# Kernel optimization log

Measured on AMD Instinct MI355X. Metric: run time of the kernel, lower is better.

Reference implementation:

```python
import jax, jax.numpy as jnp
import numpy as np

B, S, H = 2, 2048, 2048
NH, KVH, HD = 16, 4, 128
R = 16
LORA_SCALE = 32.0 / 16.0  # lora_alpha / lora_r
ATTN_SCALE = HD ** -0.5
NEG = -1e9


def setup_inputs() -> dict:
    key = jax.random.key(0)
    ks = jax.random.split(key, 16)
    q_dim, kv_dim = NH * HD, KVH * HD
    # RoPE tables
    inv_freq = 1.0 / (10000.0 ** (jnp.arange(0, HD, 2, dtype=jnp.float32) / HD))
    ang = jnp.arange(S, dtype=jnp.float32)[:, None] * inv_freq[None, :]  # [S, HD/2]
    emb = jnp.concatenate([ang, ang], axis=-1)  # [S, HD]
    cos = jnp.broadcast_to(jnp.cos(emb)[None], (B, S, HD))
    sin = jnp.broadcast_to(jnp.sin(emb)[None], (B, S, HD))
    # additive causal mask [B,1,S,S]
    causal = jnp.triu(jnp.full((S, S), NEG, dtype=jnp.float32), k=1)
    attention_mask = jnp.broadcast_to(causal[None, None], (B, 1, S, S))
    return {
        'hidden_states': jax.random.normal(ks[0], (B, S, H), jnp.float32),
        'cos': cos,
        'sin': sin,
        'attention_mask': attention_mask,
        'q_w': jax.random.normal(ks[1], (q_dim, H), jnp.float32) * 0.02,
        'k_w': jax.random.normal(ks[2], (kv_dim, H), jnp.float32) * 0.02,
        'v_w': jax.random.normal(ks[3], (kv_dim, H), jnp.float32) * 0.02,
        'q_b': jax.random.normal(ks[4], (q_dim,), jnp.float32) * 0.02,
        'k_b': jax.random.normal(ks[5], (kv_dim,), jnp.float32) * 0.02,
        'v_b': jax.random.normal(ks[6], (kv_dim,), jnp.float32) * 0.02,
        'q_A': jax.random.normal(ks[7], (H, R), jnp.float32) * (1.0 / np.sqrt(H)),
        'q_B': jax.random.normal(ks[8], (R, q_dim), jnp.float32) * 0.02,
        'k_A': jax.random.normal(ks[9], (H, R), jnp.float32) * (1.0 / np.sqrt(H)),
        'k_B': jax.random.normal(ks[10], (R, kv_dim), jnp.float32) * 0.02,
        'v_A': jax.random.normal(ks[11], (H, R), jnp.float32) * (1.0 / np.sqrt(H)),
        'v_B': jax.random.normal(ks[12], (R, kv_dim), jnp.float32) * 0.02,
        'o_w': jax.random.normal(ks[13], (H, H), jnp.float32) * 0.02,
    }


def _rotate_half(x):
    x1, x2 = x[..., : HD // 2], x[..., HD // 2:]
    return jnp.concatenate([-x2, x1], axis=-1)


def reference(hidden_states, cos, sin, attention_mask,
              q_w, k_w, v_w, q_b, k_b, v_b,
              q_A, q_B, k_A, k_B, v_A, v_B, o_w):
    x = hidden_states  # dropout p=0 (eval)
    # fused base + LoRA projections
    q = x @ q_w.T + q_b + LORA_SCALE * ((x @ q_A) @ q_B)  # [B,S,NH*HD]
    k = x @ k_w.T + k_b + LORA_SCALE * ((x @ k_A) @ k_B)  # [B,S,KVH*HD]
    v = x @ v_w.T + v_b + LORA_SCALE * ((x @ v_A) @ v_B)
    q = q.reshape(B, S, NH, HD).transpose(0, 2, 1, 3)   # [B,NH,S,HD]
    k = k.reshape(B, S, KVH, HD).transpose(0, 2, 1, 3)  # [B,KVH,S,HD]
    v = v.reshape(B, S, KVH, HD).transpose(0, 2, 1, 3)
    # RoPE
    c = cos[:, None]  # [B,1,S,HD]
    s = sin[:, None]
    q = q * c + _rotate_half(q) * s
    k = k * c + _rotate_half(k) * s
    # GQA: repeat kv heads
    n_rep = NH // KVH
    k = jnp.repeat(k, n_rep, axis=1)  # [B,NH,S,HD]
    v = jnp.repeat(v, n_rep, axis=1)
    scores = jnp.einsum('bhqd,bhkd->bhqk', q, k) * ATTN_SCALE
    scores = scores + attention_mask
    attn = jax.nn.softmax(scores.astype(jnp.float32), axis=-1).astype(q.dtype)
    out = jnp.einsum('bhqk,bhkd->bhqd', attn, v)
    out = out.transpose(0, 2, 1, 3).reshape(B, S, NH * HD)  # [B,S,H]
    return out @ o_w.T
```

## Files before the change

### kernel.cpp

```cpp
#include <hip/hip_runtime.h>

constexpr int cB   = 2;
constexpr int cS   = 2048;
constexpr int cH   = 2048;
constexpr int cNH  = 16;
constexpr int cKVH = 4;
constexpr int cHD  = 128;
constexpr int cQD  = 2048;
constexpr int cKVD = 512;
constexpr int cNQKV = 3072;
constexpr int cNTOK = 4096;
#define ATTN_SCALE 0.08838834764831845f
#define QSCALE 0.12751589549581288f

typedef __bf16 bf16;
typedef __attribute__((ext_vector_type(8))) __bf16 bf16x8;
typedef __attribute__((ext_vector_type(4))) __bf16 bf16x4;
typedef __attribute__((ext_vector_type(4))) float  f32x4;

__device__ __forceinline__ void async_load16(const bf16* g, bf16* l) {
    __builtin_amdgcn_global_load_lds(
        (const __attribute__((address_space(1))) void*)g,
        (__attribute__((address_space(3))) void*)l, 16, 0, 0);
}

__global__ void conv_f32_bf16(const float* __restrict__ in, bf16* __restrict__ out) {
    int i = (blockIdx.x * 256 + threadIdx.x) * 4;
    f32x4 v = *(const f32x4*)(in + i);
    bf16x4 o;
    o[0] = (bf16)v[0]; o[1] = (bf16)v[1]; o[2] = (bf16)v[2]; o[3] = (bf16)v[3];
    *(bf16x4*)(out + i) = o;
}

__global__ __launch_bounds__(256) void prep_w2(
        const float* __restrict__ qw, const float* __restrict__ kw, const float* __restrict__ vw,
        const float* __restrict__ qA, const float* __restrict__ qB,
        const float* __restrict__ kA, const float* __restrict__ kB,
        const float* __restrict__ vA, const float* __restrict__ vB,
        const float* __restrict__ qb, const float* __restrict__ kbias, const float* __restrict__ vb,
        bf16* __restrict__ Wc, float* __restrict__ biasc) {
    const int wave = threadIdx.x >> 6, lane = threadIdx.x & 63;
    const int n = blockIdx.y * 4 + wave;
    const int k0 = blockIdx.x * 512 + lane * 8;
    const float* W; const float* Am; const float* Bm; const float* bias; int nn, nd;
    if (n < cQD)             { W = qw; Am = qA; Bm = qB; bias = qb;    nn = n;               nd = cQD; }
    else if (n < cQD + cKVD) { W = kw; Am = kA; Bm = kB; bias = kbias; nn = n - cQD;         nd = cKVD; }
    else                     { W = vw; Am = vA; Bm = vB; bias = vb;    nn = n - cQD - cKVD;  nd = cKVD; }
    if (blockIdx.x == 0 && lane == 0) biasc[n] = bias[nn];
    float bm[16];
    #pragma unroll
    for (int r = 0; r < 16; ++r) bm[r] = Bm[r * nd + nn];
    const float* wrow = W + (size_t)nn * cH + k0;
    f32x4 w0 = *(const f32x4*)(wrow);
    f32x4 w1 = *(const f32x4*)(wrow + 4);
    bf16x8 o;
    #pragma unroll
    for (int j = 0; j < 8; ++j) {
        const f32x4* am = (const f32x4*)(Am + (size_t)(k0 + j) * 16);
        f32x4 a0 = am[0], a1 = am[1], a2 = am[2], a3 = am[3];
        float acc = 0.f;
        #pragma unroll
        for (int c = 0; c < 4; ++c) acc += a0[c] * bm[c] + a1[c] * bm[4 + c]
                                         + a2[c] * bm[8 + c] + a3[c] * bm[12 + c];
        const float wv = (j < 4) ? w0[j] : w1[j - 4];
        o[j] = (bf16)(wv + 2.0f * acc);
    }
    *(bf16x8*)&Wc[(size_t)n * cH + k0] = o;
}

__global__ __launch_bounds__(512, 2) void gemm_qkv2(const bf16* __restrict__ A, const bf16* __restrict__ Bw,
                                                    const float* __restrict__ bias,
                                                    const float* __restrict__ cosb, const float* __restrict__ sinb,
                                                    bf16* __restrict__ Qr, bf16* __restrict__ Kr,
                                                    bf16* __restrict__ Vt) {
    __shared__ bf16 Al[2][256 * 64];
    __shared__ bf16 Bl[2][256 * 64];
    const int tid = threadIdx.x;
    const int wave = tid >> 6, lane = tid & 63;
    const int quad = lane >> 4, l16 = lane & 15;
    const int wm = wave >> 2, wn = wave & 3;
    const int K = cH;
    constexpr int GX = cNQKV / 256;
    constexpr int NWG = GX * (cNTOK / 256);

    const int orig = blockIdx.y * GX + blockIdx.x;
    const int swz = (orig & 7) * (NWG >> 3) + (orig >> 3);
    const long bm = (long)(swz / GX) * 256;
    const long bn = (long)(swz % GX) * 256;

    f32x4 acc[8][4];
    #pragma unroll
    for (int i = 0; i < 8; ++i)
        #pragma unroll
        for (int j = 0; j < 4; ++j) acc[i][j] = f32x4{0.f, 0.f, 0.f, 0.f};

    int ago[4], slo[4];
    #pragma unroll
    for (int i2 = 0; i2 < 4; ++i2) {
        const int si = i2 * 512 + tid;
        const int row = si >> 3, c8 = si & 7;
        ago[i2] = row * K + (c8 ^ (row & 7)) * 8;
        slo[i2] = si * 8;
    }
    const size_t bmK = (size_t)bm * K, bnK = (size_t)bn * K;

    auto STAGE = [&](int tt, int bb) {
        const bf16* As_ = A  + bmK + (size_t)tt * 64;
        const bf16* Bs_ = Bw + bnK + (size_t)tt * 64;
        #pragma unroll
        for (int i2 = 0; i2 < 4; ++i2) {
            async_load16(As_ + ago[i2], &Al[bb][slo[i2]]);
            async_load16(Bs_ + ago[i2], &Bl[bb][slo[i2]]);
        }
    };

    constexpr int NT = cH / 64;
    STAGE(0, 0);
    STAGE(1, 1);
    const int sw = l16 & 7;
    const int arow = wm * 128 + l16;
    const int brow = (wn >> 1) * 128 + (wn & 1) * 32 + l16;

    for (int t = 0; t < NT; ++t) {
        const int buf = t & 1;
        if (t + 1 < NT) asm volatile("s_waitcnt vmcnt(8)" ::: "memory");
        else            asm volatile("s_waitcnt vmcnt(0)" ::: "memory");
        __builtin_amdgcn_s_barrier();
        const bf16* Ab = &Al[buf][0];
        const bf16* Bb = &Bl[buf][0];
        #pragma unroll
        for (int ih = 0; ih < 2; ++ih) {
            bf16x8 af[4][2];
            #pragma unroll
            for (int ii = 0; ii < 4; ++ii)
                #pragma unroll
                for (int ks = 0; ks < 2; ++ks)
                    af[ii][ks] = *(const bf16x8*)&Ab[(arow + (ih * 4 + ii) * 16) * 64 + (((ks * 4 + quad) ^ sw) * 8)];
            #pragma unroll
            for (int jh = 0; jh < 2; ++jh) {
                bf16x8 bfr[2][2];
                #pragma unroll
                for (int jj = 0; jj < 2; ++jj)
                    #pragma unroll
                    for (int ks = 0; ks < 2; ++ks)
                        bfr[jj][ks] = *(const bf16x8*)&Bb[(brow + jj * 16 + jh * 64) * 64 + (((ks * 4 + quad) ^ sw) * 8)];
                __builtin_amdgcn_s_setprio(1);
                #pragma unroll
                for (int ii = 0; ii < 4; ++ii)
                    #pragma unroll
                    for (int jj = 0; jj < 2; ++jj)
                        #pragma unroll
                        for (int ks = 0; ks < 2; ++ks)
                            acc[ih * 4 + ii][jh * 2 + jj] = __builtin_amdgcn_mfma_f32_16x16x32_bf16(
                                af[ii][ks], bfr[jj][ks], acc[ih * 4 + ii][jh * 2 + jj], 0, 0, 0);
                __builtin_amdgcn_s_setprio(0);
            }
        }
        asm volatile("s_waitcnt lgkmcnt(0)" ::: "memory");
        __builtin_amdgcn_s_barrier();
        if (t + 2 < NT) STAGE(t + 2, buf);
    }

    #pragma unroll
    for (int j = 0; j < 4; ++j) {
        const int nloc = (wn >> 1) * 128 + (wn & 1) * 32 + (j & 1) * 16 + (j >> 1) * 64 + l16;
        const float bv = bias[bn + nloc];
        #pragma unroll
        for (int i = 0; i < 8; ++i)
            #pragma unroll
            for (int r = 0; r < 4; ++r) acc[i][j][r] += bv;
    }

    const int head = (int)(bn >> 7) + (wn >> 1);
    if (head < cNH + cKVH) {
        const bool isQ = head < cNH;
        #pragma unroll
        for (int jlo = 0; jlo < 2; ++jlo) {
            const int d = (wn & 1) * 32 + jlo * 16 + l16;
            #pragma unroll
            for (int i = 0; i < 8; ++i)
                #pragma unroll
                for (int r = 0; r < 4; ++r) {
                    const long tok = bm + wm * 128 + i * 16 + quad * 4 + r;
                    const float cv = cosb[tok * cHD + d];
                    const float sv = sinb[tok * cHD + d];
                    const float v1 = acc[i][jlo][r], v2 = acc[i][jlo + 2][r];
                    float o1 = v1 * cv - v2 * sv;
                    float o2 = v2 * cv + v1 * sv;
                    if (isQ) { o1 *= QSCALE; o2 *= QSCALE; }
                    const int b = (int)(tok >> 11), s = (int)(tok & 2047);
                    bf16* dst = isQ
                        ? Qr + ((size_t)(b * cNH + head) * cS + s) * cHD
                        : Kr + ((size_t)(b * cKVH + (head - cNH)) * cS + s) * cHD;
                    dst[d]      = (bf16)o1;
                    dst[d + 64] = (bf16)o2;
                }
        }
    } else {
        const int kv = head - cNH - cKVH;
        const int b = (int)(bm >> 11);
        const int sbase = (int)(bm & 2047);
        #pragma unroll
        for (int j = 0; j < 4; ++j) {
            const int d = (wn & 1) * 32 + (j & 1) * 16 + (j >> 1) * 64 + l16;
            #pragma unroll
            for (int i = 0; i < 8; ++i) {
                const int s0 = sbase + wm * 128 + i * 16 + quad * 4;
                bf16x4 o4;
                #pragma unroll
                for (int r = 0; r < 4; ++r) o4[r] = (bf16)acc[i][j][r];
                *(bf16x4*)&Vt[((size_t)((b * cKVH + kv) * cHD) + d) * cS + s0] = o4;
            }
        }
    }
}

__global__ __launch_bounds__(512, 2) void gemm_oproj(const bf16* __restrict__ A, const bf16* __restrict__ Bw,
                                                     float* __restrict__ Cp) {
    __shared__ bf16 Al[2][256 * 64];
    __shared__ bf16 Bl[2][128 * 64];
    const int tid = threadIdx.x;
    const int wave = tid >> 6, lane = tid & 63;
    const int quad = lane >> 4, l16 = lane & 15;
    const int wm = wave >> 2, wn = wave & 3;
    constexpr int K = cH, N = cH;
    constexpr int GX = cH / 128;
    constexpr int NWG = GX * (cNTOK / 256);

    const int orig = blockIdx.y * GX + blockIdx.x;
    const int swz = (orig & 7) * (NWG >> 3) + (orig >> 3);
    const long bm = (long)(swz / GX) * 256;
    const long bn = (long)(swz % GX) * 128;

    f32x4 acc[8][2];
    #pragma unroll
    for (int i = 0; i < 8; ++i)
        #pragma unroll
        for (int j = 0; j < 2; ++j) acc[i][j] = f32x4{0.f, 0.f, 0.f, 0.f};

    int ago[4], aslo[4], bgo[2], bslo[2];
    #pragma unroll
    for (int i2 = 0; i2 < 4; ++i2) {
        const int si = i2 * 512 + tid;
        const int row = si >> 3, c8 = si & 7;
        ago[i2] = row * K + (c8 ^ (row & 7)) * 8;
        aslo[i2] = si * 8;
    }
    #pragma unroll
    for (int i2 = 0; i2 < 2; ++i2) {
        const int si = i2 * 512 + tid;
        const int row = si >> 3, c8 = si & 7;
        bgo[i2] = row * K + (c8 ^ (row & 7)) * 8;
        bslo[i2] = si * 8;
    }
    const size_t bmK = (size_t)bm * K, bnK = (size_t)bn * K;

    auto STAGE = [&](int tt, int bb) {
        const bf16* As_ = A  + bmK + (size_t)tt * 64;
        const bf16* Bs_ = Bw + bnK + (size_t)tt * 64;
        #pragma unroll
        for (int i2 = 0; i2 < 4; ++i2) async_load16(As_ + ago[i2], &Al[bb][aslo[i2]]);
        #pragma unroll
        for (int i2 = 0; i2 < 2; ++i2) async_load16(Bs_ + bgo[i2], &Bl[bb][bslo[i2]]);
    };

    constexpr int NT = K / 64;
    STAGE(0, 0);
    STAGE(1, 1);
    const int sw = l16 & 7;
    const int arow = wm * 128 + l16;
    const int brow = wn * 32 + l16;

    for (int t = 0; t < NT; ++t) {
        const int buf = t & 1;
        if (t + 1 < NT) asm volatile("s_waitcnt vmcnt(6)" ::: "memory");
        else            asm volatile("s_waitcnt vmcnt(0)" ::: "memory");
        __builtin_amdgcn_s_barrier();
        const bf16* Ab = &Al[buf][0];
        const bf16* Bb = &Bl[buf][0];
        bf16x8 bfr[2][2];
        #pragma unroll
        for (int jj = 0; jj < 2; ++jj)
            #pragma unroll
            for (int ks = 0; ks < 2; ++ks)
                bfr[jj][ks] = *(const bf16x8*)&Bb[(brow + jj * 16) * 64 + (((ks * 4 + quad) ^ sw) * 8)];
        #pragma unroll
        for (int ih = 0; ih < 2; ++ih) {
            bf16x8 af[4][2];
            #pragma unroll
            for (int ii = 0; ii < 4; ++ii)
                #pragma unroll
                for (int ks = 0; ks < 2; ++ks)
                    af[ii][ks] = *(const bf16x8*)&Ab[(arow + (ih * 4 + ii) * 16) * 64 + (((ks * 4 + quad) ^ sw) * 8)];
            __builtin_amdgcn_s_setprio(1);
            #pragma unroll
            for (int ii = 0; ii < 4; ++ii)
                #pragma unroll
                for (int jj = 0; jj < 2; ++jj)
                    #pragma unroll
                    for (int ks = 0; ks < 2; ++ks)
                        acc[ih * 4 + ii][jj] = __builtin_amdgcn_mfma_f32_16x16x32_bf16(
                            af[ii][ks], bfr[jj][ks], acc[ih * 4 + ii][jj], 0, 0, 0);
            __builtin_amdgcn_s_setprio(0);
        }
        asm volatile("s_waitcnt lgkmcnt(0)" ::: "memory");
        __builtin_amdgcn_s_barrier();
        if (t + 2 < NT) STAGE(t + 2, buf);
    }

    #pragma unroll
    for (int i = 0; i < 8; ++i)
        #pragma unroll
        for (int j = 0; j < 2; ++j) {
            const long m0 = bm + wm * 128 + i * 16 + quad * 4;
            const long n  = bn + wn * 32 + j * 16 + l16;
            #pragma unroll
            for (int r = 0; r < 4; ++r)
                Cp[(m0 + r) * N + n] = acc[i][j][r];
        }
}

__global__ __launch_bounds__(256, 2) void flash4(const bf16* __restrict__ Q, const bf16* __restrict__ K,
                                                 const bf16* __restrict__ Vt, bf16* __restrict__ Ob) {
    __shared__ bf16 kb[8192];
    __shared__ bf16 vb[8192];
    __shared__ bf16 pb[4096];
    const int tid = threadIdx.x;
    const int wave = tid >> 6, lane = tid & 63;
    const int quad = lane >> 4, l16 = lane & 15;
    const int pi = blockIdx.x;
    const int h = blockIdx.y, b = blockIdx.z;

    const bf16* Qh = Q  + (size_t)(b * cNH + h) * cS * cHD;
    const bf16* Kg = K  + (size_t)(b * cKVH + (h >> 2)) * cS * cHD;
    const bf16* Vg = Vt + (size_t)(b * cKVH + (h >> 2)) * cHD * cS;

    int kgo[4], vgo[4], slo[4];
    #pragma unroll
    for (int i2 = 0; i2 < 4; ++i2) {
        const int si = i2 * 256 + tid;
        const int krow = si >> 4, kcsw = si & 15;
        const int kc = (kcsw & 8) | ((kcsw & 7) ^ (krow & 7));
        kgo[i2] = krow * cHD + kc * 8;
        const int vrow = si >> 3, vcsw = si & 7;
        const int vc = vcsw ^ (vrow & 7);
        vgo[i2] = vrow * cS + vc * 8;
        slo[i2] = si * 8;
    }

    #pragma unroll
    for (int t2 = 0; t2 < 2; ++t2) {
        const int qt = t2 == 0 ? (31 - pi) : pi;

        const bf16* Qg = Qh + (size_t)qt * 64 * cHD;
        bf16x8 qf[4];
        #pragma unroll
        for (int ks = 0; ks < 4; ++ks)
            qf[ks] = *(const bf16x8*)(Qg + (size_t)(wave * 16 + l16) * cHD + ks * 32 + quad * 8);

        f32x4 oac[8];
        #pragma unroll
        for (int dt = 0; dt < 8; ++dt) oac[dt] = f32x4{0.f, 0.f, 0.f, 0.f};
        float m_ = -3.0e38f, l_ = 0.f;

        const int nkt = qt + 1;
        for (int kt = 0; kt < nkt; ++kt) {
            __syncthreads();
            const bf16* Kt  = Kg + (size_t)kt * 64 * cHD;
            const bf16* Vtt = Vg + kt * 64;
            #pragma unroll
            for (int i2 = 0; i2 < 4; ++i2) async_load16(Kt + kgo[i2], kb + slo[i2]);
            #pragma unroll
            for (int i2 = 0; i2 < 4; ++i2) async_load16(Vtt + vgo[i2], vb + slo[i2]);
            __syncthreads();

            f32x4 st[4];
            #pragma unroll
            for (int mt = 0; mt < 4; ++mt) {
                bf16x8 kf[4];
                #pragma unroll
                for (int ks = 0; ks < 4; ++ks) {
                    const int c = ks * 4 + quad;
                    const int csw = (c & 8) | ((c & 7) ^ (l16 & 7));
                    kf[ks] = *(const bf16x8*)&kb[(mt * 16 + l16) * 128 + csw * 8];
                }
                f32x4 a = f32x4{0.f, 0.f, 0.f, 0.f};
                #pragma unroll
                for (int ks = 0; ks < 4; ++ks)
                    a = __builtin_amdgcn_mfma_f32_16x16x32_bf16(kf[ks], qf[ks], a, 0, 0, 0);
                st[mt] = a;
            }

            const int qpos = qt * 64 + wave * 16 + l16;
            float tmax = -3.0e38f;
            if ((kt * 64 + 63) > (qt * 64 + wave * 16)) {
                #pragma unroll
                for (int mt = 0; mt < 4; ++mt)
                    #pragma unroll
                    for (int r = 0; r < 4; ++r) {
                        const int kpos = kt * 64 + mt * 16 + quad * 4 + r;
                        if (kpos > qpos) st[mt][r] = -3.0e38f;
                        tmax = fmaxf(tmax, st[mt][r]);
                    }
            } else {
                #pragma unroll
                for (int mt = 0; mt < 4; ++mt)
                    #pragma unroll
                    for (int r = 0; r < 4; ++r) tmax = fmaxf(tmax, st[mt][r]);
            }
            tmax = fmaxf(tmax, __shfl_xor(tmax, 16, 64));
            tmax = fmaxf(tmax, __shfl_xor(tmax, 32, 64));
            const float mnew = fmaxf(m_, tmax);
            if (__any(tmax > m_)) {
                const float alpha = __builtin_amdgcn_exp2f(m_ - mnew);
                l_ *= alpha;
                #pragma unroll
                for (int dt = 0; dt < 8; ++dt)
                    #pragma unroll
                    for (int r = 0; r < 4; ++r) oac[dt][r] *= alpha;
            }
            m_ = mnew;
            float rs = 0.f;
            #pragma unroll
            for (int mt = 0; mt < 4; ++mt)
                #pragma unroll
                for (int r = 0; r < 4; ++r) {
                    const float p = __builtin_amdgcn_exp2f(st[mt][r] - mnew);
                    st[mt][r] = p;
                    rs += p;
                }
            rs += __shfl_xor(rs, 16, 64);
            rs += __shfl_xor(rs, 32, 64);
            l_ += rs;

            #pragma unroll
            for (int mt = 0; mt < 4; ++mt) {
                bf16x4 p4;
                #pragma unroll
                for (int r = 0; r < 4; ++r) p4[r] = (bf16)st[mt][r];
                const int csw = (mt * 2 + (quad >> 1)) ^ (l16 & 7);
                *(bf16x4*)&pb[wave * 1024 + l16 * 64 + csw * 8 + (quad & 1) * 4] = p4;
            }

            bf16x8 pf[2];
            #pragma unroll
            for (int ks = 0; ks < 2; ++ks) {
                const int c = ks * 4 + quad;
                const int csw = c ^ (l16 & 7);
                pf[ks] = *(const bf16x8*)&pb[wave * 1024 + l16 * 64 + csw * 8];
            }
            #pragma unroll
            for (int dt = 0; dt < 8; ++dt) {
                bf16x8 vf[2];
                #pragma unroll
                for (int ks = 0; ks < 2; ++ks) {
                    const int c = ks * 4 + quad;
                    const int csw = c ^ (l16 & 7);
                    vf[ks] = *(const bf16x8*)&vb[(dt * 16 + l16) * 64 + csw * 8];
                }
                #pragma unroll
                for (int ks = 0; ks < 2; ++ks)
                    oac[dt] = __builtin_amdgcn_mfma_f32_16x16x32_bf16(vf[ks], pf[ks], oac[dt], 0, 0, 0);
            }
        }

        const float inv = 1.0f / l_;
        const int token = qt * 64 + wave * 16 + l16;
        bf16* orow = Ob + (size_t)(b * cS + token) * (cNH * cHD) + h * cHD;
        #pragma unroll
        for (int dt = 0; dt < 8; ++dt) {
            bf16x4 o4;
            #pragma unroll
            for (int r = 0; r < 4; ++r) o4[r] = (bf16)(oac[dt][r] * inv);
            *(bf16x4*)&orow[dt * 16 + quad * 4] = o4;
        }
    }
}

extern "C" void kernel_launch(void* const* d_in, const int* in_sizes, int n_in,
                              void* d_out, int out_size, void* d_ws, size_t ws_size,
                              hipStream_t stream) {
    const float* x    = (const float*)d_in[0];
    const float* cosb = (const float*)d_in[1];
    const float* sinb = (const float*)d_in[2];
    const float* qw = (const float*)d_in[4];
    const float* kw = (const float*)d_in[5];
    const float* vw = (const float*)d_in[6];
    const float* qb = (const float*)d_in[7];
    const float* kb_ = (const float*)d_in[8];
    const float* vb = (const float*)d_in[9];
    const float* qA = (const float*)d_in[10];
    const float* qB = (const float*)d_in[11];
    const float* kA = (const float*)d_in[12];
    const float* kB = (const float*)d_in[13];
    const float* vA = (const float*)d_in[14];
    const float* vB = (const float*)d_in[15];
    const float* ow = (const float*)d_in[16];
    float* out = (float*)d_out;

    char* ws = (char*)d_ws;
    bf16* Xbf   = (bf16*)ws;  ws += (size_t)cNTOK * cH * 2;
    bf16* Wc    = (bf16*)ws;  ws += (size_t)cNQKV * cH * 2;
    float* biasc = (float*)ws; ws += (size_t)cNQKV * 4;
    bf16* Qr    = (bf16*)ws;  ws += (size_t)cB * cNH * cS * cHD * 2;
    bf16* Kr    = (bf16*)ws;  ws += (size_t)cB * cKVH * cS * cHD * 2;
    bf16* Vt    = (bf16*)ws;  ws += (size_t)cB * cKVH * cHD * cS * 2;
    bf16* OWbf  = (bf16*)ws;  ws += (size_t)cH * cH * 2;
    bf16* Aout  = (bf16*)ws;  ws += (size_t)cNTOK * cQD * 2;

    conv_f32_bf16<<<(cNTOK * cH) / 1024, 256, 0, stream>>>(x, Xbf);
    conv_f32_bf16<<<(cH * cH) / 1024, 256, 0, stream>>>(ow, OWbf);
    prep_w2<<<dim3(cH / 512, cNQKV / 4), 256, 0, stream>>>(qw, kw, vw, qA, qB, kA, kB, vA, vB,
                                                           qb, kb_, vb, Wc, biasc);

    gemm_qkv2<<<dim3(cNQKV / 256, cNTOK / 256), 512, 0, stream>>>(Xbf, Wc, biasc, cosb, sinb, Qr, Kr, Vt);

    flash4<<<dim3(16, cNH, cB), 256, 0, stream>>>(Qr, Kr, Vt, Aout);

    gemm_oproj<<<dim3(cH / 128, cNTOK / 256), 512, 0, stream>>>(Aout, OWbf, out);
}
```

Baseline: 393.7 us.

## Restructure QKV GEMM main loop into quarter-tile ping-pong with interleaved async loads

Replaces the simple double-buffered K loop of the QKV projection GEMM with an 8-phase schedule per 128-wide K step. Each phase loads one quarter of the operand fragments, issues one async global-to-LDS quarter-tile load, and runs one MFMA block between barriers, so memory traffic is spread across the compute. The LDS tile is split into 64-row quarters with new row offsets. This is meant to hide global load latency and LDS stalls, at the cost of many more barriers and complex waitcnt accounting that could stall or break correctness.

```diff
diff --git a/kernel.cpp b/kernel.cpp
--- a/kernel.cpp
+++ b/kernel.cpp
@@ -68,7 +68,7 @@
     *(bf16x8*)&Wc[(size_t)n * cH + k0] = o;
 }
 
-__global__ __launch_bounds__(512, 2) void gemm_qkv2(const bf16* __restrict__ A, const bf16* __restrict__ Bw,
+__global__ __launch_bounds__(512, 2) void gemm_qkv3(const bf16* __restrict__ A, const bf16* __restrict__ Bw,
                                                     const float* __restrict__ bias,
                                                     const float* __restrict__ cosb, const float* __restrict__ sinb,
                                                     bf16* __restrict__ Qr, bf16* __restrict__ Kr,
@@ -94,72 +94,107 @@
         #pragma unroll
         for (int j = 0; j < 4; ++j) acc[i][j] = f32x4{0.f, 0.f, 0.f, 0.f};
 
-    int ago[4], slo[4];
-    #pragma unroll
-    for (int i2 = 0; i2 < 4; ++i2) {
-        const int si = i2 * 512 + tid;
-        const int row = si >> 3, c8 = si & 7;
-        ago[i2] = row * K + (c8 ^ (row & 7)) * 8;
-        slo[i2] = si * 8;
+    int gro0, gro1, lro0, lro1;
+    {
+        const int s0 = tid,        r0 = s0 >> 3, c0 = s0 & 7;
+        const int s1 = tid + 512,  r1 = s1 >> 3, c1 = s1 & 7;
+        const int R0a = (r0 >> 6) * 128 + (r0 & 63);
+        const int R0b = (r1 >> 6) * 128 + (r1 & 63);
+        gro0 = R0a * K + ((c0 ^ (R0a & 7)) * 8);
+        gro1 = R0b * K + ((c1 ^ (R0b & 7)) * 8);
+        lro0 = R0a * 64 + c0 * 8;
+        lro1 = R0b * 64 + c1 * 8;
     }
     const size_t bmK = (size_t)bm * K, bnK = (size_t)bn * K;
 
-    auto STAGE = [&](int tt, int bb) {
-        const bf16* As_ = A  + bmK + (size_t)tt * 64;
-        const bf16* Bs_ = Bw + bnK + (size_t)tt * 64;
-        #pragma unroll
-        for (int i2 = 0; i2 < 4; ++i2) {
-            async_load16(As_ + ago[i2], &Al[bb][slo[i2]]);
-            async_load16(Bs_ + ago[i2], &Bl[bb][slo[i2]]);
-        }
-    };
-
-    constexpr int NT = cH / 64;
-    STAGE(0, 0);
-    STAGE(1, 1);
+#define STG_A(Q, TT, BB) { const bf16* g_ = A + bmK + (size_t)(Q) * 64 * cH + (size_t)(TT) * 64; \
+        bf16* l_ = &Al[BB][(Q) * 4096]; \
+        async_load16(g_ + gro0, l_ + lro0); async_load16(g_ + gro1, l_ + lro1); }
+#define STG_B(Q, TT, BB) { const bf16* g_ = Bw + bnK + (size_t)(Q) * 64 * cH + (size_t)(TT) * 64; \
+        bf16* l_ = &Bl[BB][(Q) * 4096]; \
+        async_load16(g_ + gro0, l_ + lro0); async_load16(g_ + gro1, l_ + lro1); }
+
     const int sw = l16 & 7;
     const int arow = wm * 128 + l16;
     const int brow = (wn >> 1) * 128 + (wn & 1) * 32 + l16;
 
-    for (int t = 0; t < NT; ++t) {
-        const int buf = t & 1;
-        if (t + 1 < NT) asm volatile("s_waitcnt vmcnt(8)" ::: "memory");
-        else            asm volatile("s_waitcnt vmcnt(0)" ::: "memory");
-        __builtin_amdgcn_s_barrier();
-        const bf16* Ab = &Al[buf][0];
-        const bf16* Bb = &Bl[buf][0];
-        #pragma unroll
-        for (int ih = 0; ih < 2; ++ih) {
-            bf16x8 af[4][2];
-            #pragma unroll
-            for (int ii = 0; ii < 4; ++ii)
-                #pragma unroll
-                for (int ks = 0; ks < 2; ++ks)
-                    af[ii][ks] = *(const bf16x8*)&Ab[(arow + (ih * 4 + ii) * 16) * 64 + (((ks * 4 + quad) ^ sw) * 8)];
-            #pragma unroll
-            for (int jh = 0; jh < 2; ++jh) {
-                bf16x8 bfr[2][2];
-                #pragma unroll
-                for (int jj = 0; jj < 2; ++jj)
-                    #pragma unroll
-                    for (int ks = 0; ks < 2; ++ks)
-                        bfr[jj][ks] = *(const bf16x8*)&Bb[(brow + jj * 16 + jh * 64) * 64 + (((ks * 4 + quad) ^ sw) * 8)];
-                __builtin_amdgcn_s_setprio(1);
-                #pragma unroll
-                for (int ii = 0; ii < 4; ++ii)
-                    #pragma unroll
-                    for (int jj = 0; jj < 2; ++jj)
-                        #pragma unroll
-                        for (int ks = 0; ks < 2; ++ks)
-                            acc[ih * 4 + ii][jh * 2 + jj] = __builtin_amdgcn_mfma_f32_16x16x32_bf16(
-                                af[ii][ks], bfr[jj][ks], acc[ih * 4 + ii][jh * 2 + jj], 0, 0, 0);
-                __builtin_amdgcn_s_setprio(0);
-            }
-        }
-        asm volatile("s_waitcnt lgkmcnt(0)" ::: "memory");
-        __builtin_amdgcn_s_barrier();
-        if (t + 2 < NT) STAGE(t + 2, buf);
-    }
+    bf16x8 af[4][2], bfr[2][2];
+
+#define LDAF(ABP, IH) { _Pragma("unroll") for (int ii = 0; ii < 4; ++ii) \
+        _Pragma("unroll") for (int ks = 0; ks < 2; ++ks) \
+        af[ii][ks] = *(const bf16x8*)&(ABP)[(arow + ((IH) * 4 + ii) * 16) * 64 + (((ks * 4 + quad) ^ sw) * 8)]; }
+#define LDBF(BBP, JH) { _Pragma("unroll") for (int jj = 0; jj < 2; ++jj) \
+        _Pragma("unroll") for (int ks = 0; ks < 2; ++ks) \
+        bfr[jj][ks] = *(const bf16x8*)&(BBP)[(brow + jj * 16 + (JH) * 64) * 64 + (((ks * 4 + quad) ^ sw) * 8)]; }
+#define MFQ(IH, JH) { __builtin_amdgcn_s_setprio(1); \
+        _Pragma("unroll") for (int ii = 0; ii < 4; ++ii) \
+        _Pragma("unroll") for (int jj = 0; jj < 2; ++jj) \
+        _Pragma("unroll") for (int ks = 0; ks < 2; ++ks) \
+        acc[(IH) * 4 + ii][(JH) * 2 + jj] = __builtin_amdgcn_mfma_f32_16x16x32_bf16( \
+            af[ii][ks], bfr[jj][ks], acc[(IH) * 4 + ii][(JH) * 2 + jj], 0, 0, 0); \
+        __builtin_amdgcn_s_setprio(0); }
+#define PH_MID { __builtin_amdgcn_s_barrier(); asm volatile("s_waitcnt lgkmcnt(0)" ::: "memory"); }
+#define PH_END { __builtin_amdgcn_s_barrier(); }
+#define WAIT6 asm volatile("s_waitcnt vmcnt(6)" ::: "memory");
+#define WAIT0 asm volatile("s_waitcnt vmcnt(0)" ::: "memory");
+
+    const bf16* Ab0 = &Al[0][0]; const bf16* Ab1 = &Al[1][0];
+    const bf16* Bb0 = &Bl[0][0]; const bf16* Bb1 = &Bl[1][0];
+
+    constexpr int K_IT = cH / 128;
+    STG_A(0, 0, 0); STG_B(1, 0, 0); STG_A(1, 0, 0); STG_B(0, 0, 0);
+    STG_A(0, 1, 1); STG_B(1, 1, 1); STG_A(1, 1, 1);
+    WAIT6;
+    __builtin_amdgcn_s_barrier();
+
+    for (int k = 0; k < K_IT; ++k) {
+        const int t2a = 2 * k + 2, t2b = 2 * k + 3;
+        const bool more = (k + 1 < K_IT);
+        LDAF(Ab0, 0); LDBF(Bb0, 0);
+        STG_B(0, 2 * k + 1, 1);
+        PH_MID; MFQ(0, 0); PH_END;
+
+        LDBF(Bb0, 1);
+        if (more) STG_A(0, t2a, 0);
+        PH_MID; MFQ(0, 1); PH_END;
+
+        LDAF(Ab0, 1);
+        if (more) STG_B(1, t2a, 0);
+        PH_MID; MFQ(1, 1); PH_END;
+
+        LDBF(Bb0, 0);
+        if (more) STG_A(1, t2a, 0);
+        PH_MID; MFQ(1, 0);
+        if (more) { WAIT6 } else { WAIT0 }
+        PH_END;
+
+        LDAF(Ab1, 0); LDBF(Bb1, 0);
+        if (more) STG_B(0, t2a, 0);
+        PH_MID; MFQ(0, 0); PH_END;
+
+        LDBF(Bb1, 1);
+        if (more) STG_A(0, t2b, 1);
+        PH_MID; MFQ(0, 1); PH_END;
+
+        LDAF(Ab1, 1);
+        if (more) STG_B(1, t2b, 1);
+        PH_MID; MFQ(1, 1); PH_END;
+
+        LDBF(Bb1, 0);
+        if (more) STG_A(1, t2b, 1);
+        PH_MID; MFQ(1, 0);
+        if (more) { WAIT6 }
+        PH_END;
+    }
+#undef STG_A
+#undef STG_B
+#undef LDAF
+#undef LDBF
+#undef MFQ
+#undef PH_MID
+#undef PH_END
+#undef WAIT6
+#undef WAIT0
 
     #pragma unroll
     for (int j = 0; j < 4; ++j) {
@@ -513,7 +548,7 @@
     prep_w2<<<dim3(cH / 512, cNQKV / 4), 256, 0, stream>>>(qw, kw, vw, qA, qB, kA, kB, vA, vB,
                                                            qb, kb_, vb, Wc, biasc);
 
-    gemm_qkv2<<<dim3(cNQKV / 256, cNTOK / 256), 512, 0, stream>>>(Xbf, Wc, biasc, cosb, sinb, Qr, Kr, Vt);
+    gemm_qkv3<<<dim3(cNQKV / 256, cNTOK / 256), 512, 0, stream>>>(Xbf, Wc, biasc, cosb, sinb, Qr, Kr, Vt);
 
     flash4<<<dim3(16, cNH, cB), 256, 0, stream>>>(Qr, Kr, Vt, Aout);
 
```

After: 391.5 us. Within noise of the previous version (-0.6%).

## Double-buffer K/V tiles in flash attention and raise MFMA wave priority

Applied to the files above, without the earlier changes.

The flash attention kernel now keeps two LDS buffers for K and V. It issues the async global-to-LDS load for the next key tile before computing on the current one, and waits with vmcnt so the current tile is ready while the next stays in flight. The goal is to hide global load latency that was previously exposed between two syncthreads per iteration. It also wraps the MFMA sequences in s_setprio to favour matrix issue. LDS use roughly doubles for K/V, from about 40KB to about 72KB, which may limit occupancy to fewer than two blocks per CU.

```diff
diff --git a/kernel.cpp b/kernel.cpp
--- a/kernel.cpp
+++ b/kernel.cpp
@@ -320,10 +320,10 @@
         }
 }
 
-__global__ __launch_bounds__(256, 2) void flash4(const bf16* __restrict__ Q, const bf16* __restrict__ K,
+__global__ __launch_bounds__(256, 2) void flash5(const bf16* __restrict__ Q, const bf16* __restrict__ K,
                                                  const bf16* __restrict__ Vt, bf16* __restrict__ Ob) {
-    __shared__ bf16 kb[8192];
-    __shared__ bf16 vb[8192];
+    __shared__ bf16 kb[2][8192];
+    __shared__ bf16 vb[2][8192];
     __shared__ bf16 pb[4096];
     const int tid = threadIdx.x;
     const int wave = tid >> 6, lane = tid & 63;
@@ -348,6 +348,15 @@
         slo[i2] = si * 8;
     }
 
+    auto STAGE_KV = [&](int kt, int bb) {
+        const bf16* Kt  = Kg + (size_t)kt * 64 * cHD;
+        const bf16* Vtt = Vg + kt * 64;
+        #pragma unroll
+        for (int i2 = 0; i2 < 4; ++i2) async_load16(Kt + kgo[i2], &kb[bb][slo[i2]]);
+        #pragma unroll
+        for (int i2 = 0; i2 < 4; ++i2) async_load16(Vtt + vgo[i2], &vb[bb][slo[i2]]);
+    };
+
     #pragma unroll
     for (int t2 = 0; t2 < 2; ++t2) {
         const int qt = t2 == 0 ? (31 - pi) : pi;
@@ -364,15 +373,16 @@
         float m_ = -3.0e38f, l_ = 0.f;
 
         const int nkt = qt + 1;
+        STAGE_KV(0, 0);
         for (int kt = 0; kt < nkt; ++kt) {
-            __syncthreads();
-            const bf16* Kt  = Kg + (size_t)kt * 64 * cHD;
-            const bf16* Vtt = Vg + kt * 64;
-            #pragma unroll
-            for (int i2 = 0; i2 < 4; ++i2) async_load16(Kt + kgo[i2], kb + slo[i2]);
-            #pragma unroll
-            for (int i2 = 0; i2 < 4; ++i2) async_load16(Vtt + vgo[i2], vb + slo[i2]);
-            __syncthreads();
+            const int bb = kt & 1;
+            const bool more = (kt + 1 < nkt);
+            if (more) STAGE_KV(kt + 1, bb ^ 1);
+            if (more) asm volatile("s_waitcnt vmcnt(8)" ::: "memory");
+            else      asm volatile("s_waitcnt vmcnt(0)" ::: "memory");
+            __builtin_amdgcn_s_barrier();
+            const bf16* kbp = &kb[bb][0];
+            const bf16* vbp = &vb[bb][0];
 
             f32x4 st[4];
             #pragma unroll
@@ -382,12 +392,14 @@
                 for (int ks = 0; ks < 4; ++ks) {
                     const int c = ks * 4 + quad;
                     const int csw = (c & 8) | ((c & 7) ^ (l16 & 7));
-                    kf[ks] = *(const bf16x8*)&kb[(mt * 16 + l16) * 128 + csw * 8];
+                    kf[ks] = *(const bf16x8*)&kbp[(mt * 16 + l16) * 128 + csw * 8];
                 }
                 f32x4 a = f32x4{0.f, 0.f, 0.f, 0.f};
+                __builtin_amdgcn_s_setprio(1);
                 #pragma unroll
                 for (int ks = 0; ks < 4; ++ks)
                     a = __builtin_amdgcn_mfma_f32_16x16x32_bf16(kf[ks], qf[ks], a, 0, 0, 0);
+                __builtin_amdgcn_s_setprio(0);
                 st[mt] = a;
             }
 
@@ -456,12 +468,15 @@
                 for (int ks = 0; ks < 2; ++ks) {
                     const int c = ks * 4 + quad;
                     const int csw = c ^ (l16 & 7);
-                    vf[ks] = *(const bf16x8*)&vb[(dt * 16 + l16) * 64 + csw * 8];
+                    vf[ks] = *(const bf16x8*)&vbp[(dt * 16 + l16) * 64 + csw * 8];
                 }
+                __builtin_amdgcn_s_setprio(1);
                 #pragma unroll
                 for (int ks = 0; ks < 2; ++ks)
                     oac[dt] = __builtin_amdgcn_mfma_f32_16x16x32_bf16(vf[ks], pf[ks], oac[dt], 0, 0, 0);
-            }
+                __builtin_amdgcn_s_setprio(0);
+            }
+            __builtin_amdgcn_s_barrier();
         }
 
         const float inv = 1.0f / l_;
@@ -515,7 +530,7 @@
 
     gemm_qkv2<<<dim3(cNQKV / 256, cNTOK / 256), 512, 0, stream>>>(Xbf, Wc, biasc, cosb, sinb, Qr, Kr, Vt);
 
-    flash4<<<dim3(16, cNH, cB), 256, 0, stream>>>(Qr, Kr, Vt, Aout);
+    flash5<<<dim3(16, cNH, cB), 256, 0, stream>>>(Qr, Kr, Vt, Aout);
 
     gemm_oproj<<<dim3(cH / 128, cNTOK / 256), 512, 0, stream>>>(Aout, OWbf, out);
 }
```

Measured after the change: 395.3 us. No clear change (+0.4%).
